# Kernel tuning notes

Hardware: AMD Instinct MI355X
Metric: run time of the kernel (lower is better)

Reference implementation:

```python
import jax, jax.numpy as jnp
import numpy as np

N_NODES = 50000
N_EDGES = 300000
N_CLUSTERS = 100
IN_C = 256
OUT_C = 256


def setup_inputs() -> dict:
    key = jax.random.key(0)
    k1, k2, k3, k4, k5, k6 = jax.random.split(key, 6)
    X = jax.random.normal(k1, (N_NODES, IN_C), dtype=jnp.float32)
    # Cluster-GCN style block partition: contiguous clusters of equal size
    assign = ((jnp.arange(N_NODES) * N_CLUSTERS) // N_NODES).astype(jnp.int32)
    bs = N_NODES // N_CLUSTERS  # block (cluster) size
    src = jax.random.randint(k2, (N_EDGES,), 0, N_NODES)
    intra_dst = (src // bs) * bs + jax.random.randint(k3, (N_EDGES,), 0, bs)
    rand_dst = jax.random.randint(k4, (N_EDGES,), 0, N_NODES)
    dst = jnp.where(jax.random.uniform(k5, (N_EDGES,)) < 0.9, intra_dst, rand_dst)
    full_ei = jnp.stack([src, dst]).astype(jnp.int32)
    W = (jax.random.normal(k6, (IN_C, OUT_C), dtype=jnp.float32) / np.sqrt(IN_C)).astype(jnp.float32)
    b = jnp.zeros((OUT_C,), dtype=jnp.float32)
    return {"X": X, "W": W, "b": b, "assign": assign, "full_ei": full_ei}


def reference(X, W, b, assign, full_ei):
    # Equivalent to the per-cluster loop: GCNConv (add_self_loops=True, symmetric
    # normalization) applied to the subgraph of intra-cluster edges; clusters
    # with zero internal edges are skipped (nodes keep original features).
    N = X.shape[0]
    src, dst = full_ei[0], full_ei[1]
    intra = (assign[src] == assign[dst]).astype(X.dtype)  # [E]
    # per-cluster-subgraph degree, including self loop
    deg = jnp.ones((N,), X.dtype).at[dst].add(intra)  # [N]
    dis = jax.lax.rsqrt(deg)
    xW = X @ W  # [N, out_c]
    w_e = intra * dis[src] * dis[dst]  # [E]
    agg = jax.ops.segment_sum(w_e[:, None] * xW[src], dst, num_segments=N)
    agg = agg + xW / deg[:, None]  # self-loop term: norm = 1/deg
    out = agg + b
    has_edge = jax.ops.segment_sum(intra, assign[src], num_segments=N_CLUSTERS) > 0
    return jnp.where(has_edge[assign][:, None], out, X)
```

## Files before the change

kernel.cpp:

```cpp
#include <hip/hip_runtime.h>
#include <hip/hip_bf16.h>

#define N_NODES 50000
#define N_EDGES 300000
#define N_CLUSTERS 100
#define CH 256
#define CAP 32

typedef __attribute__((ext_vector_type(8))) short short8;
typedef __attribute__((ext_vector_type(4))) float f32x4;

static __device__ inline unsigned short f2bf(float f) {
    unsigned int u = __float_as_uint(f);
    u += 0x7fffu + ((u >> 16) & 1u);
    return (unsigned short)(u >> 16);
}


__global__ void init_kernel(int* __restrict__ indeg, int* __restrict__ flags) {
    int i = blockIdx.x * blockDim.x + threadIdx.x;
    if (i < N_NODES) indeg[i] = 0;
    if (i < N_CLUSTERS) flags[i] = 0;
}

__global__ void scatter_kernel(const int* __restrict__ ei, const int* __restrict__ assign,
                               int* __restrict__ indeg, int* __restrict__ flags,
                               int* __restrict__ csr) {
    int e = blockIdx.x * blockDim.x + threadIdx.x;
    if (e >= N_EDGES) return;
    int s = ei[e], d = ei[N_EDGES + e];
    int cs = assign[s];
    if (cs == assign[d]) {
        int p = atomicAdd(&indeg[d], 1);
        if (p < CAP) csr[d * CAP + p] = s;
        flags[cs] = 1;
    }
}

__global__ void convw_kernel(const float* __restrict__ W, unsigned short* __restrict__ Wt) {
    int n = blockIdx.x, k = threadIdx.x;
    Wt[n * CH + k] = f2bf(W[k * CH + n]);
}


#define BM 64
#define BK 32
#define LDSS 40

__global__ __launch_bounds__(256, 3) void gemm_bf16(const float* __restrict__ X,
                                                    const unsigned short* __restrict__ Wt,
                                                    unsigned short* __restrict__ xWb) {
    __shared__ unsigned short Xs[BM * LDSS];
    __shared__ unsigned short Ws[CH * LDSS];
    int tid = threadIdx.x;
    int row0 = blockIdx.x * BM;
    int wid = tid >> 6, lane = tid & 63;
    int wn = wid * 64;
    int l15 = lane & 15, quad = lane >> 4;

    f32x4 acc[4][4] = {};

    int srow = tid >> 2;
    int skc  = (tid & 3) * 8;
    int garow = row0 + srow; if (garow >= N_NODES) garow = N_NODES - 1;
    const float* gA = X + (size_t)garow * CH + skc;
    unsigned short* lA = &Xs[srow * LDSS + skc];
    const unsigned short* gB = Wt + (size_t)tid * CH;
    unsigned short* lB = &Ws[tid * LDSS];

    for (int k0 = 0; k0 < CH; k0 += BK) {
        float4 x0 = *reinterpret_cast<const float4*>(gA + k0);
        float4 x1 = *reinterpret_cast<const float4*>(gA + k0 + 4);
        uint4 b0 = *reinterpret_cast<const uint4*>(gB + k0);
        uint4 b1 = *reinterpret_cast<const uint4*>(gB + k0 + 8);
        uint4 b2 = *reinterpret_cast<const uint4*>(gB + k0 + 16);
        uint4 b3 = *reinterpret_cast<const uint4*>(gB + k0 + 24);
        ushort4 a0 = { f2bf(x0.x), f2bf(x0.y), f2bf(x0.z), f2bf(x0.w) };
        ushort4 a1 = { f2bf(x1.x), f2bf(x1.y), f2bf(x1.z), f2bf(x1.w) };
        *reinterpret_cast<ushort4*>(lA)     = a0;
        *reinterpret_cast<ushort4*>(lA + 4) = a1;
        *reinterpret_cast<uint4*>(lB)      = b0;
        *reinterpret_cast<uint4*>(lB + 8)  = b1;
        *reinterpret_cast<uint4*>(lB + 16) = b2;
        *reinterpret_cast<uint4*>(lB + 24) = b3;
        __syncthreads();

        short8 af[4], bf[4];
#pragma unroll
        for (int mi = 0; mi < 4; ++mi)
            af[mi] = *reinterpret_cast<const short8*>(
                &Xs[(mi * 16 + l15) * LDSS + quad * 8]);
#pragma unroll
        for (int ni = 0; ni < 4; ++ni)
            bf[ni] = *reinterpret_cast<const short8*>(
                &Ws[(wn + ni * 16 + l15) * LDSS + quad * 8]);
#pragma unroll
        for (int mi = 0; mi < 4; ++mi)
#pragma unroll
            for (int ni = 0; ni < 4; ++ni)
                acc[mi][ni] = __builtin_amdgcn_mfma_f32_16x16x32_bf16(
                    af[mi], bf[ni], acc[mi][ni], 0, 0, 0);
        __syncthreads();
    }

#pragma unroll
    for (int mi = 0; mi < 4; ++mi)
#pragma unroll
        for (int r = 0; r < 4; ++r) {
            int grow = row0 + mi * 16 + quad * 4 + r;
            if (grow < N_NODES) {
                size_t rb = (size_t)grow * CH + wn + l15;
#pragma unroll
                for (int ni = 0; ni < 4; ++ni)
                    xWb[rb + ni * 16] = f2bf(acc[mi][ni][r]);
            }
        }
}


#define NBLK ((N_NODES + 3) / 4)
#define BLK_PER_XCD ((NBLK + 7) / 8)

static __device__ inline void bf4_fma(float w, uint2 v, float& ax, float& ay, float& az, float& aw) {
    ax += w * __uint_as_float(v.x << 16);
    ay += w * __uint_as_float(v.x & 0xffff0000u);
    az += w * __uint_as_float(v.y << 16);
    aw += w * __uint_as_float(v.y & 0xffff0000u);
}

__global__ __launch_bounds__(256) void gather_kernel(const unsigned short* __restrict__ xWb,
        const float* __restrict__ X, const float* __restrict__ b,
        const int* __restrict__ assign, const int* __restrict__ flags,
        const int* __restrict__ indeg, const int* __restrict__ csr,
        float* __restrict__ out) {
    int blk = (blockIdx.x & 7) * BLK_PER_XCD + (blockIdx.x >> 3);
    if (blk >= NBLK) return;
    int node = blk * 4 + (threadIdx.x >> 6);
    int lane = threadIdx.x & 63;
    if (node >= N_NODES) return;
    float4* out4 = reinterpret_cast<float4*>(out);
    size_t base4 = (size_t)node * 64 + lane;
    if (flags[assign[node]] == 0) {
        out4[base4] = reinterpret_cast<const float4*>(X)[base4];
        return;
    }
    int cnt_raw = indeg[node];
    int cnt = cnt_raw > CAP ? CAP : cnt_raw;
    float dn = rsqrtf(1.0f + (float)cnt_raw);

    int   s_l = 0;
    float w_l = 0.0f;
    if (lane < cnt) {
        s_l = csr[node * CAP + lane];
        w_l = rsqrtf(1.0f + (float)indeg[s_l]) * dn;
    }

    float selfw = dn * dn;
    uint2 sv = *reinterpret_cast<const uint2*>(xWb + (size_t)node * CH + lane * 4);
    float ax = 0, ay = 0, az = 0, aw = 0;
    bf4_fma(selfw, sv, ax, ay, az, aw);

    int i = 0;
    for (; i + 4 <= cnt; i += 4) {
        int   s0 = __shfl(s_l, i),     s1 = __shfl(s_l, i + 1);
        int   s2 = __shfl(s_l, i + 2), s3 = __shfl(s_l, i + 3);
        float w0 = __shfl(w_l, i),     w1 = __shfl(w_l, i + 1);
        float w2 = __shfl(w_l, i + 2), w3 = __shfl(w_l, i + 3);
        uint2 v0 = *reinterpret_cast<const uint2*>(xWb + (size_t)s0 * CH + lane * 4);
        uint2 v1 = *reinterpret_cast<const uint2*>(xWb + (size_t)s1 * CH + lane * 4);
        uint2 v2 = *reinterpret_cast<const uint2*>(xWb + (size_t)s2 * CH + lane * 4);
        uint2 v3 = *reinterpret_cast<const uint2*>(xWb + (size_t)s3 * CH + lane * 4);
        bf4_fma(w0, v0, ax, ay, az, aw);
        bf4_fma(w1, v1, ax, ay, az, aw);
        bf4_fma(w2, v2, ax, ay, az, aw);
        bf4_fma(w3, v3, ax, ay, az, aw);
    }
    for (; i < cnt; ++i) {
        int   s = __shfl(s_l, i);
        float w = __shfl(w_l, i);
        uint2 v = *reinterpret_cast<const uint2*>(xWb + (size_t)s * CH + lane * 4);
        bf4_fma(w, v, ax, ay, az, aw);
    }

    float4 bb = reinterpret_cast<const float4*>(b)[lane];
    float4 o = { ax + bb.x, ay + bb.y, az + bb.z, aw + bb.w };
    out4[base4] = o;
}


extern "C" void kernel_launch(void* const* d_in, const int* in_sizes, int n_in,
                              void* d_out, int out_size, void* d_ws, size_t ws_size,
                              hipStream_t stream) {
    const float* X      = (const float*)d_in[0];
    const float* W      = (const float*)d_in[1];
    const float* b      = (const float*)d_in[2];
    const int*   assign = (const int*)d_in[3];
    const int*   ei     = (const int*)d_in[4];
    float* out = (float*)d_out;

    char* ws = (char*)d_ws;
    size_t off = 0;
    auto alloc = [&](size_t bytes) -> void* {
        void* p = ws + off;
        off = (off + bytes + 255) & ~(size_t)255;
        return p;
    };
    unsigned short* xWb = (unsigned short*)alloc((size_t)N_NODES * CH * sizeof(unsigned short));
    unsigned short* Wt  = (unsigned short*)alloc((size_t)CH * CH * sizeof(unsigned short));
    int*   csr   = (int*)alloc((size_t)N_NODES * CAP * sizeof(int));
    int*   indeg = (int*)alloc(N_NODES * sizeof(int));
    int*   flags = (int*)alloc(N_CLUSTERS * sizeof(int));
    (void)ws_size; (void)n_in; (void)in_sizes; (void)out_size;

    init_kernel<<<(N_NODES + 255) / 256, 256, 0, stream>>>(indeg, flags);
    scatter_kernel<<<(N_EDGES + 255) / 256, 256, 0, stream>>>(ei, assign, indeg, flags, csr);
    convw_kernel<<<CH, CH, 0, stream>>>(W, Wt);
    gemm_bf16<<<(N_NODES + BM - 1) / BM, 256, 0, stream>>>(X, Wt, xWb);
    gather_kernel<<<BLK_PER_XCD * 8, 256, 0, stream>>>(xWb, X, b, assign, flags, indeg,
                                                       csr, out);
}
```

Baseline: 176.6 us.

## Keep W fragments in registers and stage full-K X tile once in GEMM

The GEMM now loads each wave's full B (W) fragments into registers up front and stages the entire 64x256 X tile into LDS once with a single barrier. This removes the per-K-step LDS staging of W and the repeated barriers. In exchange it uses far more registers, so launch bounds drop to 2 blocks per SM. Separately, the gather loop pads the neighbour count to a multiple of four and drops the scalar tail loop. Padded slots rely on lanes beyond cnt holding s=0 and w=0, so they load node 0's row and multiply it by zero.

```diff
diff --git a/kernel.cpp b/kernel.cpp
--- a/kernel.cpp
+++ b/kernel.cpp
@@ -44,63 +44,61 @@
 
 
 #define BM 64
-#define BK 32
-#define LDSS 40
-
-__global__ __launch_bounds__(256, 3) void gemm_bf16(const float* __restrict__ X,
+#define ALDS 264
+
+__global__ __launch_bounds__(256, 2) void gemm_bf16(const float* __restrict__ X,
                                                     const unsigned short* __restrict__ Wt,
                                                     unsigned short* __restrict__ xWb) {
-    __shared__ unsigned short Xs[BM * LDSS];
-    __shared__ unsigned short Ws[CH * LDSS];
+    __shared__ unsigned short Xs[BM * ALDS];
     int tid = threadIdx.x;
     int row0 = blockIdx.x * BM;
     int wid = tid >> 6, lane = tid & 63;
     int wn = wid * 64;
     int l15 = lane & 15, quad = lane >> 4;
 
+    short8 breg[4][8];
+#pragma unroll
+    for (int ni = 0; ni < 4; ++ni) {
+        const unsigned short* p = Wt + (size_t)(wn + ni * 16 + l15) * CH + quad * 8;
+#pragma unroll
+        for (int c = 0; c < 8; ++c)
+            breg[ni][c] = *reinterpret_cast<const short8*>(p + c * 32);
+    }
+
+    int srow = tid >> 2;
+    int scol = (tid & 3) * 64;
+    int garow = row0 + srow; if (garow >= N_NODES) garow = N_NODES - 1;
+    const float* gA = X + (size_t)garow * CH + scol;
+    unsigned short* lA = &Xs[srow * ALDS + scol];
+#pragma unroll
+    for (int j = 0; j < 16; j += 2) {
+        float4 u = *reinterpret_cast<const float4*>(gA + j * 4);
+        float4 v = *reinterpret_cast<const float4*>(gA + j * 4 + 4);
+        ushort4 lo = { f2bf(u.x), f2bf(u.y), f2bf(u.z), f2bf(u.w) };
+        ushort4 hi = { f2bf(v.x), f2bf(v.y), f2bf(v.z), f2bf(v.w) };
+        uint4 packed;
+        packed.x = (unsigned)lo.x | ((unsigned)lo.y << 16);
+        packed.y = (unsigned)lo.z | ((unsigned)lo.w << 16);
+        packed.z = (unsigned)hi.x | ((unsigned)hi.y << 16);
+        packed.w = (unsigned)hi.z | ((unsigned)hi.w << 16);
+        *reinterpret_cast<uint4*>(lA + j * 4) = packed;
+    }
+    __syncthreads();
+
     f32x4 acc[4][4] = {};
-
-    int srow = tid >> 2;
-    int skc  = (tid & 3) * 8;
-    int garow = row0 + srow; if (garow >= N_NODES) garow = N_NODES - 1;
-    const float* gA = X + (size_t)garow * CH + skc;
-    unsigned short* lA = &Xs[srow * LDSS + skc];
-    const unsigned short* gB = Wt + (size_t)tid * CH;
-    unsigned short* lB = &Ws[tid * LDSS];
-
-    for (int k0 = 0; k0 < CH; k0 += BK) {
-        float4 x0 = *reinterpret_cast<const float4*>(gA + k0);
-        float4 x1 = *reinterpret_cast<const float4*>(gA + k0 + 4);
-        uint4 b0 = *reinterpret_cast<const uint4*>(gB + k0);
-        uint4 b1 = *reinterpret_cast<const uint4*>(gB + k0 + 8);
-        uint4 b2 = *reinterpret_cast<const uint4*>(gB + k0 + 16);
-        uint4 b3 = *reinterpret_cast<const uint4*>(gB + k0 + 24);
-        ushort4 a0 = { f2bf(x0.x), f2bf(x0.y), f2bf(x0.z), f2bf(x0.w) };
-        ushort4 a1 = { f2bf(x1.x), f2bf(x1.y), f2bf(x1.z), f2bf(x1.w) };
-        *reinterpret_cast<ushort4*>(lA)     = a0;
-        *reinterpret_cast<ushort4*>(lA + 4) = a1;
-        *reinterpret_cast<uint4*>(lB)      = b0;
-        *reinterpret_cast<uint4*>(lB + 8)  = b1;
-        *reinterpret_cast<uint4*>(lB + 16) = b2;
-        *reinterpret_cast<uint4*>(lB + 24) = b3;
-        __syncthreads();
-
-        short8 af[4], bf[4];
+#pragma unroll
+    for (int c = 0; c < 8; ++c) {
+        short8 af[4];
 #pragma unroll
         for (int mi = 0; mi < 4; ++mi)
             af[mi] = *reinterpret_cast<const short8*>(
-                &Xs[(mi * 16 + l15) * LDSS + quad * 8]);
-#pragma unroll
-        for (int ni = 0; ni < 4; ++ni)
-            bf[ni] = *reinterpret_cast<const short8*>(
-                &Ws[(wn + ni * 16 + l15) * LDSS + quad * 8]);
+                &Xs[(mi * 16 + l15) * ALDS + c * 32 + quad * 8]);
 #pragma unroll
         for (int mi = 0; mi < 4; ++mi)
 #pragma unroll
             for (int ni = 0; ni < 4; ++ni)
                 acc[mi][ni] = __builtin_amdgcn_mfma_f32_16x16x32_bf16(
-                    af[mi], bf[ni], acc[mi][ni], 0, 0, 0);
-        __syncthreads();
+                    af[mi], breg[ni][c], acc[mi][ni], 0, 0, 0);
     }
 
 #pragma unroll
@@ -160,8 +158,8 @@
     float ax = 0, ay = 0, az = 0, aw = 0;
     bf4_fma(selfw, sv, ax, ay, az, aw);
 
-    int i = 0;
-    for (; i + 4 <= cnt; i += 4) {
+    int cnt4 = (cnt + 3) & ~3;
+    for (int i = 0; i < cnt4; i += 4) {
         int   s0 = __shfl(s_l, i),     s1 = __shfl(s_l, i + 1);
         int   s2 = __shfl(s_l, i + 2), s3 = __shfl(s_l, i + 3);
         float w0 = __shfl(w_l, i),     w1 = __shfl(w_l, i + 1);
@@ -174,12 +172,6 @@
         bf4_fma(w1, v1, ax, ay, az, aw);
         bf4_fma(w2, v2, ax, ay, az, aw);
         bf4_fma(w3, v3, ax, ay, az, aw);
-    }
-    for (; i < cnt; ++i) {
-        int   s = __shfl(s_l, i);
-        float w = __shfl(w_l, i);
-        uint2 v = *reinterpret_cast<const uint2*>(xWb + (size_t)s * CH + lane * 4);
-        bf4_fma(w, v, ax, ay, az, aw);
     }
 
     float4 bb = reinterpret_cast<const float4*>(b)[lane];
```

New measurement: 174.9 us. No clear change (-1.0%).
